# Kernel tuning notes

Hardware: AMD Instinct MI355X
Metric: run time of the kernel (lower is better)

The kernel has to match this reference:

```python
import jax, jax.numpy as jnp
import numpy as np

N = 100000
E = 800000
H = 4          # heads
C = 64         # per-head channels (concat=False -> head-mean, out dim 64)
G = 2000       # number of graphs
NEG_SLOPE = 0.2


def setup_inputs() -> dict:
    key = jax.random.key(0)
    ks = jax.random.split(key, 16)
    x = jax.random.normal(ks[0], (N, 9), dtype=jnp.float32)
    edge_index = jax.random.randint(ks[1], (2, E), 0, N, dtype=jnp.int64)
    batch = jnp.sort(jax.random.randint(ks[2], (N,), 0, G, dtype=jnp.int64))
    s = 0.1
    params = {}
    in_dims = [9, C, C]
    for l in range(3):
        kw, kas, kad = jax.random.split(ks[3 + l], 3)
        params[f'W{l+1}'] = jax.random.normal(kw, (in_dims[l], H * C), dtype=jnp.float32) * s
        params[f'as{l+1}'] = jax.random.normal(kas, (H, C), dtype=jnp.float32) * s
        params[f'ad{l+1}'] = jax.random.normal(kad, (H, C), dtype=jnp.float32) * s
        params[f'b{l+1}'] = jnp.zeros((C,), dtype=jnp.float32)
    params['lin_w'] = jax.random.normal(ks[7], (C, 1), dtype=jnp.float32) * s
    params['lin_b'] = jnp.zeros((1,), dtype=jnp.float32)
    return {'x': x, 'edge_index': edge_index, 'batch': batch, **params}


def _gat_conv(x, src, dst, W, a_src, a_dst, b):
    # x: [N, F_in] -> h: [N, H, C]
    h = (x @ W).reshape(N, H, C)
    al_s = jnp.einsum('nhc,hc->nh', h, a_src)   # [N, H]
    al_d = jnp.einsum('nhc,hc->nh', h, a_dst)   # [N, H]
    e = jax.nn.leaky_relu(al_s[src] + al_d[dst], NEG_SLOPE)  # [E+, H]
    # segment softmax over incoming edges of each dst node
    m = jax.ops.segment_max(e, dst, num_segments=N)
    ex = jnp.exp(e - m[dst])
    denom = jax.ops.segment_sum(ex, dst, num_segments=N)
    alpha = ex / (denom[dst] + 1e-16)            # [E+, H]
    msg = h[src] * alpha[:, :, None]             # [E+, H, C]
    out = jax.ops.segment_sum(msg, dst, num_segments=N)  # [N, H, C]
    return out.mean(axis=1) + b                  # concat=False -> head mean + bias


def reference(x, edge_index, batch, W1, as1, ad1, b1, W2, as2, ad2, b2,
              W3, as3, ad3, b3, lin_w, lin_b):
    # PyG GATConv adds self-loops by default
    loops = jnp.arange(N, dtype=edge_index.dtype)
    src = jnp.concatenate([edge_index[0], loops])
    dst = jnp.concatenate([edge_index[1], loops])

    h = jax.nn.relu(_gat_conv(x, src, dst, W1, as1, ad1, b1))
    h = jax.nn.relu(_gat_conv(h, src, dst, W2, as2, ad2, b2))
    h = jax.nn.relu(_gat_conv(h, src, dst, W3, as3, ad3, b3))

    # global_mean_pool over graphs
    sums = jax.ops.segment_sum(h, batch, num_segments=G)            # [G, C]
    cnts = jax.ops.segment_sum(jnp.ones((N,), h.dtype), batch, num_segments=G)
    pooled = sums / jnp.maximum(cnts, 1.0)[:, None]
    return pooled @ lin_w + lin_b                                    # [G, 1]
```

## Files before the change

kernel.cpp:

```cpp
#include <hip/hip_runtime.h>
#include <hip/hip_bf16.h>

#define NN 100000
#define EE 800000
#define HH 4
#define CC 64
#define GG 2000
#define NB 98

typedef unsigned short ushortx;
typedef __attribute__((ext_vector_type(8))) short short8;
typedef __attribute__((ext_vector_type(4))) float f32x4;


__global__ void hist_kernel(const int* __restrict__ ei, int* __restrict__ deg,
                            int* __restrict__ rank) {
    int e = blockIdx.x * 256 + threadIdx.x;
    const int tot = EE + NN;
    if (e < tot) {
        int d = (e < EE) ? ei[EE + e] : (e - EE);
        rank[e] = atomicAdd(&deg[d], 1);
    }
}

__global__ __launch_bounds__(256) void scan_blk(const int* __restrict__ deg,
                                                int* __restrict__ bsum) {
    const int t = threadIdx.x;
    const int idx4 = blockIdx.x * 256 + t;
    int4 v = {0, 0, 0, 0};
    if (idx4 < NN / 4) v = ((const int4*)deg)[idx4];
    int s = v.x + v.y + v.z + v.w;
#pragma unroll
    for (int m = 32; m; m >>= 1) s += __shfl_xor(s, m, 64);
    __shared__ int ws[4];
    if ((t & 63) == 0) ws[t >> 6] = s;
    __syncthreads();
    if (t == 0) bsum[blockIdx.x] = ws[0] + ws[1] + ws[2] + ws[3];
}

__global__ void scan_mid(const int* __restrict__ bsum, int* __restrict__ boff,
                         int* __restrict__ off) {
    __shared__ int sh[128];
    const int t = threadIdx.x;
    int v = (t < NB) ? bsum[t] : 0;
    sh[t] = v;
    __syncthreads();
    for (int d = 1; d < 128; d <<= 1) {
        int u = (t >= d) ? sh[t - d] : 0;
        __syncthreads();
        sh[t] += u;
        __syncthreads();
    }
    if (t < NB) boff[t] = sh[t] - v;
    if (t == NB - 1) off[NN] = sh[t];
}

__global__ __launch_bounds__(256) void scan_fin(const int* __restrict__ deg,
                                                const int* __restrict__ boff,
                                                int* __restrict__ off) {
    const int t = threadIdx.x;
    const int idx4 = blockIdx.x * 256 + t;
    int4 v = {0, 0, 0, 0};
    if (idx4 < NN / 4) v = ((const int4*)deg)[idx4];
    int s = v.x + v.y + v.z + v.w;
    const int lane = t & 63, w = t >> 6;
    int inc = s;
#pragma unroll
    for (int d = 1; d < 64; d <<= 1) {
        int u = __shfl_up(inc, d, 64);
        if (lane >= d) inc += u;
    }
    __shared__ int ws[4];
    if (lane == 63) ws[w] = inc;
    __syncthreads();
    int woff = 0;
    for (int i = 0; i < w; ++i) woff += ws[i];
    int excl = inc - s + woff + boff[blockIdx.x];
    if (idx4 < NN / 4) {
        int4 o;
        o.x = excl;
        o.y = o.x + v.x;
        o.z = o.y + v.y;
        o.w = o.z + v.z;
        ((int4*)off)[idx4] = o;
    }
}

__global__ __launch_bounds__(256) void fill_sharded(
    const int* __restrict__ ei, const int* __restrict__ off,
    const int* __restrict__ rank, int* __restrict__ csr_src) {
    const int shard = blockIdx.x & 7;
    const int wblk = blockIdx.x >> 3;
    const int lo = shard * (NN / 8);
    const int hi = lo + (NN / 8);
    const int tot = EE + NN;
    for (int e = wblk * 256 + threadIdx.x; e < tot; e += 256 * 256) {
        int d = (e < EE) ? ei[EE + e] : (e - EE);
        if (d >= lo && d < hi) {
            int s = (e < EE) ? ei[e] : (e - EE);
            csr_src[off[d] + rank[e]] = s;
        }
    }
}

__device__ __forceinline__ ushortx f2bf(float v) {
    __hip_bfloat16 b = __float2bfloat16(v);
    return *reinterpret_cast<ushortx*>(&b);
}


__device__ __forceinline__ void do_va(const float* __restrict__ W,
                                      const float* __restrict__ as_,
                                      const float* __restrict__ ad_,
                                      float* __restrict__ va, int K, int id) {
    if (id >= K * 8) return;
    int k = id >> 3, comp = id & 7;
    int h = comp & 3, sd = comp >> 2;
    const float* a = sd ? ad_ : as_;
    const float* wrow = W + k * 256 + h * 64;
    const float* arow = a + h * 64;
    float s = 0.f;
    for (int c = 0; c < 64; ++c) s = fmaf(wrow[c], arow[c], s);
    va[k * 8 + comp] = s;
}

__device__ __forceinline__ void do_wfrag(const float* __restrict__ W,
                                         ushortx* __restrict__ wfrag, int i) {
    if (i >= 16384) return;
    int j = i & 7, lane = (i >> 3) & 63, kb = (i >> 9) & 7, ct = i >> 12;
    int c = ct * 16 + (lane & 15);
    int kap = kb * 32 + (lane >> 4) * 8 + j;
    int h = kap >> 6, kw = kap & 63;
    wfrag[i] = f2bf(W[kw * 256 + h * 64 + c] * 0.25f);
}

__global__ void prep_all(
    const float* __restrict__ W1, const float* __restrict__ as1,
    const float* __restrict__ ad1, const float* __restrict__ W2,
    const float* __restrict__ as2, const float* __restrict__ ad2,
    const float* __restrict__ W3, const float* __restrict__ as3,
    const float* __restrict__ ad3, float* __restrict__ va1,
    float* __restrict__ va2, float* __restrict__ va3,
    ushortx* __restrict__ wf2, ushortx* __restrict__ wf3) {
    const int b = blockIdx.x, tid = threadIdx.x;
    if (b == 0) do_va(W1, as1, ad1, va1, 9, tid);
    else if (b <= 2) do_va(W2, as2, ad2, va2, 64, (b - 1) * 256 + tid);
    else if (b <= 4) do_va(W3, as3, ad3, va3, 64, (b - 3) * 256 + tid);
    else if (b <= 68) do_wfrag(W2, wf2, (b - 5) * 256 + tid);
    else do_wfrag(W3, wf3, (b - 69) * 256 + tid);
}

template <int K>
__global__ __launch_bounds__(256) void att_gemv(
    const float* __restrict__ X, const float* __restrict__ va,
    float* __restrict__ ALS, float* __restrict__ ALD) {
    __shared__ float vs[K][8];
    const int tid = threadIdx.x;
    for (int i = tid; i < K * 8; i += 256) vs[i >> 3][i & 7] = va[i];
    __syncthreads();
    int n = blockIdx.x * 256 + tid;
    if (n >= NN) return;
    const float* xp = X + (size_t)n * K;
    float s0 = 0, s1 = 0, s2 = 0, s3 = 0, d0 = 0, d1 = 0, d2 = 0, d3 = 0;
#pragma unroll
    for (int k = 0; k < K; ++k) {
        float x1 = xp[k];
        const float4 vsv = *(const float4*)&vs[k][0];
        const float4 vdv = *(const float4*)&vs[k][4];
        s0 = fmaf(x1, vsv.x, s0); s1 = fmaf(x1, vsv.y, s1);
        s2 = fmaf(x1, vsv.z, s2); s3 = fmaf(x1, vsv.w, s3);
        d0 = fmaf(x1, vdv.x, d0); d1 = fmaf(x1, vdv.y, d1);
        d2 = fmaf(x1, vdv.z, d2); d3 = fmaf(x1, vdv.w, d3);
    }
    float4 so = {s0, s1, s2, s3}, dd = {d0, d1, d2, d3};
    ((float4*)ALS)[n] = so;
    ((float4*)ALD)[n] = dd;
}

__global__ __launch_bounds__(256) void att_gemv_b(
    const ushortx* __restrict__ Xb, const float* __restrict__ va,
    float* __restrict__ ALS, float* __restrict__ ALD) {
    __shared__ float vs[64][8];
    const int tid = threadIdx.x;
    for (int i = tid; i < 64 * 8; i += 256) vs[i >> 3][i & 7] = va[i];
    __syncthreads();
    int n = blockIdx.x * 256 + tid;
    if (n >= NN) return;
    const uint4* xp = (const uint4*)(Xb + (size_t)n * 64);
    float s0 = 0, s1 = 0, s2 = 0, s3 = 0, d0 = 0, d1 = 0, d2 = 0, d3 = 0;
#pragma unroll
    for (int qq = 0; qq < 8; ++qq) {
        uint4 u = xp[qq];
        float xv[8];
        xv[0] = __uint_as_float(u.x << 16);
        xv[1] = __uint_as_float(u.x & 0xFFFF0000u);
        xv[2] = __uint_as_float(u.y << 16);
        xv[3] = __uint_as_float(u.y & 0xFFFF0000u);
        xv[4] = __uint_as_float(u.z << 16);
        xv[5] = __uint_as_float(u.z & 0xFFFF0000u);
        xv[6] = __uint_as_float(u.w << 16);
        xv[7] = __uint_as_float(u.w & 0xFFFF0000u);
#pragma unroll
        for (int j = 0; j < 8; ++j) {
            const int k = qq * 8 + j;
            const float4 vsv = *(const float4*)&vs[k][0];
            const float4 vdv = *(const float4*)&vs[k][4];
            s0 = fmaf(xv[j], vsv.x, s0); s1 = fmaf(xv[j], vsv.y, s1);
            s2 = fmaf(xv[j], vsv.z, s2); s3 = fmaf(xv[j], vsv.w, s3);
            d0 = fmaf(xv[j], vdv.x, d0); d1 = fmaf(xv[j], vdv.y, d1);
            d2 = fmaf(xv[j], vdv.z, d2); d3 = fmaf(xv[j], vdv.w, d3);
        }
    }
    float4 so = {s0, s1, s2, s3}, dd = {d0, d1, d2, d3};
    ((float4*)ALS)[n] = so;
    ((float4*)ALD)[n] = dd;
}

__device__ __forceinline__ float4 edge_w4(const float4 a, const float4 aldv) {
    float vx = a.x + aldv.x, vy = a.y + aldv.y,
          vz = a.z + aldv.z, vw = a.w + aldv.w;
    vx = (vx >= 0.f) ? vx : 0.2f * vx;
    vy = (vy >= 0.f) ? vy : 0.2f * vy;
    vz = (vz >= 0.f) ? vz : 0.2f * vz;
    vw = (vw >= 0.f) ? vw : 0.2f * vw;
    float4 w;
    w.x = __expf(vx); w.y = __expf(vy); w.z = __expf(vz); w.w = __expf(vw);
    return w;
}


__global__ __launch_bounds__(256) void agg_gemm1(
    const float* __restrict__ X, const float* __restrict__ ALS,
    const float* __restrict__ ALD, const int* __restrict__ off,
    const int* __restrict__ csr_src, const float* __restrict__ W1,
    const float* __restrict__ b1, ushortx* __restrict__ Xb) {
    __shared__ float4 wtab4[4][4][21];
    __shared__ int    svtab[4][4][21];
    __shared__ float  sX[16][40];
    const int wv = threadIdx.x >> 6;
    const int l = threadIdx.x & 63;
    const int g = l >> 4, kg = l & 15;
    const int node = blockIdx.x * 16 + wv * 4 + g;
    const bool act = (kg < 9);
    const int beg = off[node], end = off[node + 1];
    int md = end - beg;
    md = max(md, __shfl_xor(md, 16, 64));
    md = max(md, __shfl_xor(md, 32, 64));
    const float4 aldv = ((const float4*)ALD)[node];
    const float4* wt = &wtab4[wv][g][0];
    const int* st = &svtab[wv][g][0];
    float4 acc = {0.f, 0.f, 0.f, 0.f};
    float4 den4 = {0.f, 0.f, 0.f, 0.f};

    for (int c0 = 0; c0 < md; c0 += 16) {
        const int jj = beg + c0 + kg;
        int sv = 0;
        float4 w4 = {0.f, 0.f, 0.f, 0.f};
        if (jj < end) {
            sv = csr_src[jj];
            w4 = edge_w4(((const float4*)ALS)[sv], aldv);
        }
        den4.x += w4.x; den4.y += w4.y; den4.z += w4.z; den4.w += w4.w;
        wtab4[wv][g][kg] = w4;
        svtab[wv][g][kg] = sv;
        __builtin_amdgcn_wave_barrier();
        asm volatile("s_waitcnt lgkmcnt(0)" ::: "memory");
        __builtin_amdgcn_sched_barrier(0);

        const int mc = min(16, md - c0);
        for (int t = 0; t < mc; t += 4) {
            float4 wA = wt[t + 0]; int sA = st[t + 0];
            float4 wB = wt[t + 1]; int sB = st[t + 1];
            float4 wC = wt[t + 2]; int sC = st[t + 2];
            float4 wD = wt[t + 3]; int sD = st[t + 3];
            float vA = 0.f, vB = 0.f, vC = 0.f, vD = 0.f;
            if (act) {
                vA = X[(size_t)sA * 9 + kg];
                vB = X[(size_t)sB * 9 + kg];
                vC = X[(size_t)sC * 9 + kg];
                vD = X[(size_t)sD * 9 + kg];
            }
            acc.x = fmaf(wA.x, vA, acc.x); acc.y = fmaf(wA.y, vA, acc.y);
            acc.z = fmaf(wA.z, vA, acc.z); acc.w = fmaf(wA.w, vA, acc.w);
            acc.x = fmaf(wB.x, vB, acc.x); acc.y = fmaf(wB.y, vB, acc.y);
            acc.z = fmaf(wB.z, vB, acc.z); acc.w = fmaf(wB.w, vB, acc.w);
            acc.x = fmaf(wC.x, vC, acc.x); acc.y = fmaf(wC.y, vC, acc.y);
            acc.z = fmaf(wC.z, vC, acc.z); acc.w = fmaf(wC.w, vC, acc.w);
            acc.x = fmaf(wD.x, vD, acc.x); acc.y = fmaf(wD.y, vD, acc.y);
            acc.z = fmaf(wD.z, vD, acc.z); acc.w = fmaf(wD.w, vD, acc.w);
        }
        __builtin_amdgcn_wave_barrier();
    }

#pragma unroll
    for (int m = 1; m <= 8; m <<= 1) {
        den4.x += __shfl_xor(den4.x, m, 64);
        den4.y += __shfl_xor(den4.y, m, 64);
        den4.z += __shfl_xor(den4.z, m, 64);
        den4.w += __shfl_xor(den4.w, m, 64);
    }
    if (act) {
        float i0 = 1.f / (den4.x + 1e-16f);
        float i1 = 1.f / (den4.y + 1e-16f);
        float i2 = 1.f / (den4.z + 1e-16f);
        float i3 = 1.f / (den4.w + 1e-16f);
        float* o = &sX[wv * 4 + g][0];
        o[0 * 9 + kg] = acc.x * i0;
        o[1 * 9 + kg] = acc.y * i1;
        o[2 * 9 + kg] = acc.z * i2;
        o[3 * 9 + kg] = acc.w * i3;
    }
    __syncthreads();

    const int c = l;
    float wreg[36];
#pragma unroll
    for (int h = 0; h < 4; ++h)
#pragma unroll
        for (int k = 0; k < 9; ++k)
            wreg[h * 9 + k] = W1[k * 256 + h * 64 + c] * 0.25f;
    const float bc = b1[c];
#pragma unroll
    for (int r = 0; r < 4; ++r) {
        const int row = wv * 4 + r;
        float s = 0.f;
#pragma unroll
        for (int i4 = 0; i4 < 9; ++i4) {
            const float4 xv = *(const float4*)&sX[row][i4 * 4];
            s = fmaf(wreg[i4 * 4 + 0], xv.x, s);
            s = fmaf(wreg[i4 * 4 + 1], xv.y, s);
            s = fmaf(wreg[i4 * 4 + 2], xv.z, s);
            s = fmaf(wreg[i4 * 4 + 3], xv.w, s);
        }
        s = fmaxf(s + bc, 0.f);
        Xb[(size_t)(blockIdx.x * 16 + row) * 64 + c] = f2bf(s);
    }
}


template <bool F32OUT>
__global__ __launch_bounds__(256) void agg_gemm(
    const ushortx* __restrict__ Xb, const float* __restrict__ ALS,
    const float* __restrict__ ALD, const int* __restrict__ off,
    const int* __restrict__ csr_src, const ushortx* __restrict__ wfrag,
    const float* __restrict__ bias, ushortx* __restrict__ XbOut,
    float* __restrict__ OUTF) {
    __shared__ float4 wtab4[4][4][21];
    __shared__ int    svtab[4][4][21];
    __shared__ ushortx sAgg[16][264];
    const int wv = threadIdx.x >> 6;
    const int l = threadIdx.x & 63;
    const int g = l >> 4, c4 = l & 15;
    const int node = blockIdx.x * 16 + wv * 4 + g;
    const int beg = off[node], end = off[node + 1];
    int md = end - beg;
    md = max(md, __shfl_xor(md, 16, 64));
    md = max(md, __shfl_xor(md, 32, 64));
    const float4 aldv = ((const float4*)ALD)[node];
    const uint2* xb2 = (const uint2*)Xb;
    const float4* wt = &wtab4[wv][g][0];
    const int* st = &svtab[wv][g][0];
    float4 a0 = {0.f, 0.f, 0.f, 0.f};
    float4 a1 = {0.f, 0.f, 0.f, 0.f};
    float4 a2 = {0.f, 0.f, 0.f, 0.f};
    float4 a3 = {0.f, 0.f, 0.f, 0.f};
    float4 den4 = {0.f, 0.f, 0.f, 0.f};

#define UPD(uu, ww)                                                 \
    {                                                               \
        float c0v = __uint_as_float((uu).x << 16);                  \
        float c1v = __uint_as_float((uu).x & 0xFFFF0000u);          \
        float c2v = __uint_as_float((uu).y << 16);                  \
        float c3v = __uint_as_float((uu).y & 0xFFFF0000u);          \
        a0.x = fmaf((ww).x, c0v, a0.x); a0.y = fmaf((ww).x, c1v, a0.y); \
        a0.z = fmaf((ww).x, c2v, a0.z); a0.w = fmaf((ww).x, c3v, a0.w); \
        a1.x = fmaf((ww).y, c0v, a1.x); a1.y = fmaf((ww).y, c1v, a1.y); \
        a1.z = fmaf((ww).y, c2v, a1.z); a1.w = fmaf((ww).y, c3v, a1.w); \
        a2.x = fmaf((ww).z, c0v, a2.x); a2.y = fmaf((ww).z, c1v, a2.y); \
        a2.z = fmaf((ww).z, c2v, a2.z); a2.w = fmaf((ww).z, c3v, a2.w); \
        a3.x = fmaf((ww).w, c0v, a3.x); a3.y = fmaf((ww).w, c1v, a3.y); \
        a3.z = fmaf((ww).w, c2v, a3.z); a3.w = fmaf((ww).w, c3v, a3.w); \
    }

    for (int c0 = 0; c0 < md; c0 += 16) {
        const int jj = beg + c0 + c4;
        int sv = 0;
        float4 w4 = {0.f, 0.f, 0.f, 0.f};
        if (jj < end) {
            sv = csr_src[jj];
            w4 = edge_w4(((const float4*)ALS)[sv], aldv);
        }
        den4.x += w4.x; den4.y += w4.y; den4.z += w4.z; den4.w += w4.w;
        wtab4[wv][g][c4] = w4;
        svtab[wv][g][c4] = sv;
        __builtin_amdgcn_wave_barrier();
        asm volatile("s_waitcnt lgkmcnt(0)" ::: "memory");
        __builtin_amdgcn_sched_barrier(0);

        const int mc = min(16, md - c0);
        for (int t = 0; t < mc; t += 4) {
            float4 wA = wt[t + 0]; int sA = st[t + 0];
            float4 wB = wt[t + 1]; int sB = st[t + 1];
            float4 wC = wt[t + 2]; int sC = st[t + 2];
            float4 wD = wt[t + 3]; int sD = st[t + 3];
            uint2 uA = xb2[(size_t)sA * 16 + c4];
            uint2 uB = xb2[(size_t)sB * 16 + c4];
            uint2 uC = xb2[(size_t)sC * 16 + c4];
            uint2 uD = xb2[(size_t)sD * 16 + c4];
            UPD(uA, wA);
            UPD(uB, wB);
            UPD(uC, wC);
            UPD(uD, wD);
        }
        __builtin_amdgcn_wave_barrier();
    }
#undef UPD

#pragma unroll
    for (int m = 1; m <= 8; m <<= 1) {
        den4.x += __shfl_xor(den4.x, m, 64);
        den4.y += __shfl_xor(den4.y, m, 64);
        den4.z += __shfl_xor(den4.z, m, 64);
        den4.w += __shfl_xor(den4.w, m, 64);
    }
    {
        float i0 = 1.f / (den4.x + 1e-16f);
        float i1 = 1.f / (den4.y + 1e-16f);
        float i2 = 1.f / (den4.z + 1e-16f);
        float i3 = 1.f / (den4.w + 1e-16f);
        ushortx* orow = &sAgg[wv * 4 + g][0];
        uint p0, p1;
        p0 = (uint)f2bf(a0.x * i0) | ((uint)f2bf(a0.y * i0) << 16);
        p1 = (uint)f2bf(a0.z * i0) | ((uint)f2bf(a0.w * i0) << 16);
        *(uint2*)&orow[0 * 64 + c4 * 4] = uint2{p0, p1};
        p0 = (uint)f2bf(a1.x * i1) | ((uint)f2bf(a1.y * i1) << 16);
        p1 = (uint)f2bf(a1.z * i1) | ((uint)f2bf(a1.w * i1) << 16);
        *(uint2*)&orow[1 * 64 + c4 * 4] = uint2{p0, p1};
        p0 = (uint)f2bf(a2.x * i2) | ((uint)f2bf(a2.y * i2) << 16);
        p1 = (uint)f2bf(a2.z * i2) | ((uint)f2bf(a2.w * i2) << 16);
        *(uint2*)&orow[2 * 64 + c4 * 4] = uint2{p0, p1};
        p0 = (uint)f2bf(a3.x * i3) | ((uint)f2bf(a3.y * i3) << 16);
        p1 = (uint)f2bf(a3.z * i3) | ((uint)f2bf(a3.w * i3) << 16);
        *(uint2*)&orow[3 * 64 + c4 * 4] = uint2{p0, p1};
    }
    __syncthreads();

    const int n = l & 15, q = l >> 4;
    f32x4 acc = {0.f, 0.f, 0.f, 0.f};
#pragma unroll
    for (int kb = 0; kb < 8; ++kb) {
        short8 a = *(const short8*)&sAgg[n][kb * 32 + q * 8];
        short8 b = *(const short8*)&wfrag[(size_t)((wv * 8 + kb) * 64 + l) * 8];
        acc = __builtin_amdgcn_mfma_f32_16x16x32_bf16(b, a, acc, 0, 0, 0);
    }
    const int row = blockIdx.x * 16 + n;
    const int col = wv * 16 + q * 4;
    float4 b4 = ((const float4*)bias)[wv * 4 + q];
    float o0 = fmaxf(acc[0] + b4.x, 0.f);
    float o1 = fmaxf(acc[1] + b4.y, 0.f);
    float o2 = fmaxf(acc[2] + b4.z, 0.f);
    float o3 = fmaxf(acc[3] + b4.w, 0.f);
    if constexpr (F32OUT) {
        float4 ov = {o0, o1, o2, o3};
        *(float4*)&OUTF[(size_t)row * 64 + col] = ov;
    } else {
        uint p0 = (uint)f2bf(o0) | ((uint)f2bf(o1) << 16);
        uint p1 = (uint)f2bf(o2) | ((uint)f2bf(o3) << 16);
        uint2 ov = {p0, p1};
        *(uint2*)&XbOut[(size_t)row * 64 + col] = ov;
    }
}


__global__ __launch_bounds__(256) void pool_graph(
    const float* __restrict__ OUTF, const int* __restrict__ batch,
    const float* __restrict__ lw, const float* __restrict__ lb,
    float* __restrict__ out) {
    const int g = blockIdx.x * 4 + (threadIdx.x >> 6);
    const int l = threadIdx.x & 63;
    if (g >= GG) return;
    int lo = 0, hi = NN;
    while (lo < hi) { int mid = (lo + hi) >> 1; if (batch[mid] < g) lo = mid + 1; else hi = mid; }
    int lo2 = lo, hi2 = NN;
    while (lo2 < hi2) { int mid = (lo2 + hi2) >> 1; if (batch[mid] < g + 1) lo2 = mid + 1; else hi2 = mid; }
    float s = 0.f;
    int nn = lo;
    for (; nn + 4 <= lo2; nn += 4) {
        float a0 = OUTF[(size_t)(nn + 0) * 64 + l];
        float a1 = OUTF[(size_t)(nn + 1) * 64 + l];
        float a2 = OUTF[(size_t)(nn + 2) * 64 + l];
        float a3 = OUTF[(size_t)(nn + 3) * 64 + l];
        s += (a0 + a1) + (a2 + a3);
    }
    for (; nn < lo2; ++nn) s += OUTF[(size_t)nn * 64 + l];
    const float cntf = fmaxf((float)(lo2 - lo), 1.f);
    float v = s / cntf * lw[l];
#pragma unroll
    for (int m = 32; m; m >>= 1) v += __shfl_xor(v, m, 64);
    if (l == 0) out[g] = v + lb[0];
}


extern "C" void kernel_launch(void* const* d_in, const int* in_sizes, int n_in,
                              void* d_out, int out_size, void* d_ws, size_t ws_size,
                              hipStream_t stream) {
    const float* x     = (const float*)d_in[0];
    const int*   ei    = (const int*)d_in[1];
    const int*   batch = (const int*)d_in[2];
    const float* W1  = (const float*)d_in[3];
    const float* as1 = (const float*)d_in[4];
    const float* ad1 = (const float*)d_in[5];
    const float* b1  = (const float*)d_in[6];
    const float* W2  = (const float*)d_in[7];
    const float* as2 = (const float*)d_in[8];
    const float* ad2 = (const float*)d_in[9];
    const float* b2  = (const float*)d_in[10];
    const float* W3  = (const float*)d_in[11];
    const float* as3 = (const float*)d_in[12];
    const float* ad3 = (const float*)d_in[13];
    const float* b3  = (const float*)d_in[14];
    const float* lw  = (const float*)d_in[15];
    const float* lb  = (const float*)d_in[16];
    float* out = (float*)d_out;

    char* p = (char*)d_ws;
    auto carve = [&](size_t bytes) -> void* {
        void* r = (void*)p;
        p += (bytes + 255) & ~(size_t)255;
        return r;
    };
    int*     off    = (int*)carve((NN + 4) * sizeof(int));
    int*     deg    = (int*)carve(NN * sizeof(int));
    int*     rank   = (int*)carve((size_t)(EE + NN) * sizeof(int));
    int*     bsum   = (int*)carve(NB * sizeof(int));
    int*     boff   = (int*)carve(NB * sizeof(int));
    int*     csr    = (int*)carve((size_t)(EE + NN) * sizeof(int));
    ushortx* xb1    = (ushortx*)carve((size_t)NN * 64 * sizeof(ushortx));
    ushortx* xb2    = (ushortx*)carve((size_t)NN * 64 * sizeof(ushortx));
    float*   outf   = (float*)carve((size_t)NN * 64 * sizeof(float));
    float*   als    = (float*)carve((size_t)NN * 4 * sizeof(float));
    float*   ald    = (float*)carve((size_t)NN * 4 * sizeof(float));
    float*   va1    = (float*)carve(9 * 8 * sizeof(float));
    float*   va2    = (float*)carve(64 * 8 * sizeof(float));
    float*   va3    = (float*)carve(64 * 8 * sizeof(float));
    ushortx* wf2    = (ushortx*)carve(16384 * sizeof(ushortx));
    ushortx* wf3    = (ushortx*)carve(16384 * sizeof(ushortx));

    hipMemsetAsync(deg, 0, NN * sizeof(int), stream);

    const int etot = EE + NN;
    const int eblocks = (etot + 255) / 256;
    hist_kernel<<<eblocks, 256, 0, stream>>>(ei, deg, rank);
    scan_blk<<<NB, 256, 0, stream>>>(deg, bsum);
    scan_mid<<<1, 128, 0, stream>>>(bsum, boff, off);
    scan_fin<<<NB, 256, 0, stream>>>(deg, boff, off);
    fill_sharded<<<2048, 256, 0, stream>>>(ei, off, rank, csr);

    prep_all<<<133, 256, 0, stream>>>(W1, as1, ad1, W2, as2, ad2, W3, as3, ad3,
                                      va1, va2, va3, wf2, wf3);

    const int ablocks = NN / 16;
    const int nblocks = (NN + 255) / 256;

    att_gemv<9><<<nblocks, 256, 0, stream>>>(x, va1, als, ald);
    agg_gemm1<<<ablocks, 256, 0, stream>>>(x, als, ald, off, csr, W1, b1, xb1);

    att_gemv_b<<<nblocks, 256, 0, stream>>>(xb1, va2, als, ald);
    agg_gemm<false><<<ablocks, 256, 0, stream>>>(xb1, als, ald, off, csr, wf2,
                                                 b2, xb2, nullptr);

    att_gemv_b<<<nblocks, 256, 0, stream>>>(xb2, va3, als, ald);
    agg_gemm<true><<<ablocks, 256, 0, stream>>>(xb2, als, ald, off, csr, wf3,
                                                b3, nullptr, outf);

    pool_graph<<<(GG + 3) / 4, 256, 0, stream>>>(outf, batch, lw, lb, out);
}
```

Measured before the change: 292.0 us.

## Fuse next-layer attention GEMV into aggregation kernel epilogues

Removes the two standalone att_gemv_b launches. Each aggregation kernel now computes the next layer's per-node source and destination attention logits in its epilogue, from the freshly produced bf16 outputs, using shuffles and a small shared reduction. The ALS/ALD buffers are double-buffered so a kernel can read the current logits while writing the next ones. This saves re-reading the 100k x 64 bf16 features and two kernel launches, at the cost of extra epilogue work and an added syncthreads.

```diff
diff --git a/kernel.cpp b/kernel.cpp
--- a/kernel.cpp
+++ b/kernel.cpp
@@ -177,45 +177,6 @@
     ((float4*)ALD)[n] = dd;
 }
 
-__global__ __launch_bounds__(256) void att_gemv_b(
-    const ushortx* __restrict__ Xb, const float* __restrict__ va,
-    float* __restrict__ ALS, float* __restrict__ ALD) {
-    __shared__ float vs[64][8];
-    const int tid = threadIdx.x;
-    for (int i = tid; i < 64 * 8; i += 256) vs[i >> 3][i & 7] = va[i];
-    __syncthreads();
-    int n = blockIdx.x * 256 + tid;
-    if (n >= NN) return;
-    const uint4* xp = (const uint4*)(Xb + (size_t)n * 64);
-    float s0 = 0, s1 = 0, s2 = 0, s3 = 0, d0 = 0, d1 = 0, d2 = 0, d3 = 0;
-#pragma unroll
-    for (int qq = 0; qq < 8; ++qq) {
-        uint4 u = xp[qq];
-        float xv[8];
-        xv[0] = __uint_as_float(u.x << 16);
-        xv[1] = __uint_as_float(u.x & 0xFFFF0000u);
-        xv[2] = __uint_as_float(u.y << 16);
-        xv[3] = __uint_as_float(u.y & 0xFFFF0000u);
-        xv[4] = __uint_as_float(u.z << 16);
-        xv[5] = __uint_as_float(u.z & 0xFFFF0000u);
-        xv[6] = __uint_as_float(u.w << 16);
-        xv[7] = __uint_as_float(u.w & 0xFFFF0000u);
-#pragma unroll
-        for (int j = 0; j < 8; ++j) {
-            const int k = qq * 8 + j;
-            const float4 vsv = *(const float4*)&vs[k][0];
-            const float4 vdv = *(const float4*)&vs[k][4];
-            s0 = fmaf(xv[j], vsv.x, s0); s1 = fmaf(xv[j], vsv.y, s1);
-            s2 = fmaf(xv[j], vsv.z, s2); s3 = fmaf(xv[j], vsv.w, s3);
-            d0 = fmaf(xv[j], vdv.x, d0); d1 = fmaf(xv[j], vdv.y, d1);
-            d2 = fmaf(xv[j], vdv.z, d2); d3 = fmaf(xv[j], vdv.w, d3);
-        }
-    }
-    float4 so = {s0, s1, s2, s3}, dd = {d0, d1, d2, d3};
-    ((float4*)ALS)[n] = so;
-    ((float4*)ALD)[n] = dd;
-}
-
 __device__ __forceinline__ float4 edge_w4(const float4 a, const float4 aldv) {
     float vx = a.x + aldv.x, vy = a.y + aldv.y,
           vz = a.z + aldv.z, vw = a.w + aldv.w;
@@ -233,10 +194,13 @@
     const float* __restrict__ X, const float* __restrict__ ALS,
     const float* __restrict__ ALD, const int* __restrict__ off,
     const int* __restrict__ csr_src, const float* __restrict__ W1,
-    const float* __restrict__ b1, ushortx* __restrict__ Xb) {
+    const float* __restrict__ b1, ushortx* __restrict__ Xb,
+    const float* __restrict__ va_next, float* __restrict__ ALSo,
+    float* __restrict__ ALDo) {
     __shared__ float4 wtab4[4][4][21];
     __shared__ int    svtab[4][4][21];
     __shared__ float  sX[16][40];
+    __shared__ float  sOut[16][68];
     const int wv = threadIdx.x >> 6;
     const int l = threadIdx.x & 63;
     const int g = l >> 4, kg = l & 15;
@@ -333,21 +297,55 @@
             s = fmaf(wreg[i4 * 4 + 3], xv.w, s);
         }
         s = fmaxf(s + bc, 0.f);
-        Xb[(size_t)(blockIdx.x * 16 + row) * 64 + c] = f2bf(s);
-    }
-}
-
-
-template <bool F32OUT>
+        ushortx bb = f2bf(s);
+        Xb[(size_t)(blockIdx.x * 16 + row) * 64 + c] = bb;
+        sOut[row][c] = __uint_as_float((uint)bb << 16);
+    }
+    __syncthreads();
+
+    const int rr = threadIdx.x >> 4, pp = threadIdx.x & 15;
+    const float4 vv = *(const float4*)&sOut[rr][pp * 4];
+    float pa0 = 0, pa1 = 0, pa2 = 0, pa3 = 0, pa4 = 0, pa5 = 0, pa6 = 0, pa7 = 0;
+#pragma unroll
+    for (int j = 0; j < 4; ++j) {
+        const int cc = pp * 4 + j;
+        const float v = (j == 0) ? vv.x : (j == 1) ? vv.y : (j == 2) ? vv.z : vv.w;
+        const float4 vsv = *(const float4*)&va_next[cc * 8];
+        const float4 vdv = *(const float4*)&va_next[cc * 8 + 4];
+        pa0 = fmaf(v, vsv.x, pa0); pa1 = fmaf(v, vsv.y, pa1);
+        pa2 = fmaf(v, vsv.z, pa2); pa3 = fmaf(v, vsv.w, pa3);
+        pa4 = fmaf(v, vdv.x, pa4); pa5 = fmaf(v, vdv.y, pa5);
+        pa6 = fmaf(v, vdv.z, pa6); pa7 = fmaf(v, vdv.w, pa7);
+    }
+#pragma unroll
+    for (int m = 1; m <= 8; m <<= 1) {
+        pa0 += __shfl_xor(pa0, m, 64); pa1 += __shfl_xor(pa1, m, 64);
+        pa2 += __shfl_xor(pa2, m, 64); pa3 += __shfl_xor(pa3, m, 64);
+        pa4 += __shfl_xor(pa4, m, 64); pa5 += __shfl_xor(pa5, m, 64);
+        pa6 += __shfl_xor(pa6, m, 64); pa7 += __shfl_xor(pa7, m, 64);
+    }
+    if (pp == 0) {
+        const int node2 = blockIdx.x * 16 + rr;
+        float4 so4 = {pa0, pa1, pa2, pa3};
+        float4 do4 = {pa4, pa5, pa6, pa7};
+        ((float4*)ALSo)[node2] = so4;
+        ((float4*)ALDo)[node2] = do4;
+    }
+}
+
+
+template <bool LAST>
 __global__ __launch_bounds__(256) void agg_gemm(
     const ushortx* __restrict__ Xb, const float* __restrict__ ALS,
     const float* __restrict__ ALD, const int* __restrict__ off,
     const int* __restrict__ csr_src, const ushortx* __restrict__ wfrag,
     const float* __restrict__ bias, ushortx* __restrict__ XbOut,
-    float* __restrict__ OUTF) {
+    float* __restrict__ OUTF, const float* __restrict__ va_next,
+    float* __restrict__ ALSo, float* __restrict__ ALDo) {
     __shared__ float4 wtab4[4][4][21];
     __shared__ int    svtab[4][4][21];
     __shared__ ushortx sAgg[16][264];
+    __shared__ float  pred[4][16][10];
     const int wv = threadIdx.x >> 6;
     const int l = threadIdx.x & 63;
     const int g = l >> 4, c4 = l & 15;
@@ -460,7 +458,7 @@
     float o1 = fmaxf(acc[1] + b4.y, 0.f);
     float o2 = fmaxf(acc[2] + b4.z, 0.f);
     float o3 = fmaxf(acc[3] + b4.w, 0.f);
-    if constexpr (F32OUT) {
+    if constexpr (LAST) {
         float4 ov = {o0, o1, o2, o3};
         *(float4*)&OUTF[(size_t)row * 64 + col] = ov;
     } else {
@@ -468,6 +466,46 @@
         uint p1 = (uint)f2bf(o2) | ((uint)f2bf(o3) << 16);
         uint2 ov = {p0, p1};
         *(uint2*)&XbOut[(size_t)row * 64 + col] = ov;
+
+        float v0 = __uint_as_float(p0 << 16);
+        float v1 = __uint_as_float(p0 & 0xFFFF0000u);
+        float v2 = __uint_as_float(p1 << 16);
+        float v3 = __uint_as_float(p1 & 0xFFFF0000u);
+        float pa0 = 0, pa1 = 0, pa2 = 0, pa3 = 0;
+        float pa4 = 0, pa5 = 0, pa6 = 0, pa7 = 0;
+#pragma unroll
+        for (int j = 0; j < 4; ++j) {
+            const float v = (j == 0) ? v0 : (j == 1) ? v1 : (j == 2) ? v2 : v3;
+            const float4 vsv = *(const float4*)&va_next[(col + j) * 8];
+            const float4 vdv = *(const float4*)&va_next[(col + j) * 8 + 4];
+            pa0 = fmaf(v, vsv.x, pa0); pa1 = fmaf(v, vsv.y, pa1);
+            pa2 = fmaf(v, vsv.z, pa2); pa3 = fmaf(v, vsv.w, pa3);
+            pa4 = fmaf(v, vdv.x, pa4); pa5 = fmaf(v, vdv.y, pa5);
+            pa6 = fmaf(v, vdv.z, pa6); pa7 = fmaf(v, vdv.w, pa7);
+        }
+        pa0 += __shfl_xor(pa0, 16, 64); pa0 += __shfl_xor(pa0, 32, 64);
+        pa1 += __shfl_xor(pa1, 16, 64); pa1 += __shfl_xor(pa1, 32, 64);
+        pa2 += __shfl_xor(pa2, 16, 64); pa2 += __shfl_xor(pa2, 32, 64);
+        pa3 += __shfl_xor(pa3, 16, 64); pa3 += __shfl_xor(pa3, 32, 64);
+        pa4 += __shfl_xor(pa4, 16, 64); pa4 += __shfl_xor(pa4, 32, 64);
+        pa5 += __shfl_xor(pa5, 16, 64); pa5 += __shfl_xor(pa5, 32, 64);
+        pa6 += __shfl_xor(pa6, 16, 64); pa6 += __shfl_xor(pa6, 32, 64);
+        pa7 += __shfl_xor(pa7, 16, 64); pa7 += __shfl_xor(pa7, 32, 64);
+        if (l < 16) {
+            pred[wv][l][0] = pa0; pred[wv][l][1] = pa1;
+            pred[wv][l][2] = pa2; pred[wv][l][3] = pa3;
+            pred[wv][l][4] = pa4; pred[wv][l][5] = pa5;
+            pred[wv][l][6] = pa6; pred[wv][l][7] = pa7;
+        }
+        __syncthreads();
+        if (threadIdx.x < 128) {
+            const int rr = threadIdx.x >> 3, k = threadIdx.x & 7;
+            const float v = (pred[0][rr][k] + pred[1][rr][k]) +
+                            (pred[2][rr][k] + pred[3][rr][k]);
+            const int node2 = blockIdx.x * 16 + rr;
+            if (k < 4) ALSo[node2 * 4 + k] = v;
+            else       ALDo[node2 * 4 + (k - 4)] = v;
+        }
     }
 }
 
@@ -538,8 +576,10 @@
     ushortx* xb1    = (ushortx*)carve((size_t)NN * 64 * sizeof(ushortx));
     ushortx* xb2    = (ushortx*)carve((size_t)NN * 64 * sizeof(ushortx));
     float*   outf   = (float*)carve((size_t)NN * 64 * sizeof(float));
-    float*   als    = (float*)carve((size_t)NN * 4 * sizeof(float));
-    float*   ald    = (float*)carve((size_t)NN * 4 * sizeof(float));
+    float*   alsA   = (float*)carve((size_t)NN * 4 * sizeof(float));
+    float*   aldA   = (float*)carve((size_t)NN * 4 * sizeof(float));
+    float*   alsB   = (float*)carve((size_t)NN * 4 * sizeof(float));
+    float*   aldB   = (float*)carve((size_t)NN * 4 * sizeof(float));
     float*   va1    = (float*)carve(9 * 8 * sizeof(float));
     float*   va2    = (float*)carve(64 * 8 * sizeof(float));
     float*   va3    = (float*)carve(64 * 8 * sizeof(float));
@@ -562,16 +602,17 @@
     const int ablocks = NN / 16;
     const int nblocks = (NN + 255) / 256;
 
-    att_gemv<9><<<nblocks, 256, 0, stream>>>(x, va1, als, ald);
-    agg_gemm1<<<ablocks, 256, 0, stream>>>(x, als, ald, off, csr, W1, b1, xb1);
-
-    att_gemv_b<<<nblocks, 256, 0, stream>>>(xb1, va2, als, ald);
-    agg_gemm<false><<<ablocks, 256, 0, stream>>>(xb1, als, ald, off, csr, wf2,
-                                                 b2, xb2, nullptr);
-
-    att_gemv_b<<<nblocks, 256, 0, stream>>>(xb2, va3, als, ald);
-    agg_gemm<true><<<ablocks, 256, 0, stream>>>(xb2, als, ald, off, csr, wf3,
-                                                b3, nullptr, outf);
+    att_gemv<9><<<nblocks, 256, 0, stream>>>(x, va1, alsA, aldA);
+    agg_gemm1<<<ablocks, 256, 0, stream>>>(x, alsA, aldA, off, csr, W1, b1,
+                                           xb1, va2, alsB, aldB);
+
+    agg_gemm<false><<<ablocks, 256, 0, stream>>>(xb1, alsB, aldB, off, csr,
+                                                 wf2, b2, xb2, nullptr, va3,
+                                                 alsA, aldA);
+
+    agg_gemm<true><<<ablocks, 256, 0, stream>>>(xb2, alsA, aldA, off, csr,
+                                                wf3, b3, nullptr, outf,
+                                                nullptr, nullptr, nullptr);
 
     pool_graph<<<(GG + 3) / 4, 256, 0, stream>>>(outf, batch, lw, lb, out);
 }
```

Result: slower. 302.1 us (+3.5%).
